# Kernel tuning notes

Measured on AMD Instinct MI355X. Metric: run time of the kernel, lower is better.

The kernel has to match this reference:

```python
import jax, jax.numpy as jnp
import numpy as np
import math

# (n, m) pairs used in forward: n in range(min(max_order,4)) = 0..3, m in -n..n step 2, (n-|m|)%2==0 -> 10 pairs
PAIRS = [(n, m) for n in range(4) for m in range(-n, n + 1, 2) if (n - abs(m)) % 2 == 0]
NPAIR = len(PAIRS)  # 10
MAXP = 3  # max radial power for n <= 3
_Cmat = np.zeros((NPAIR, MAXP + 1), dtype=np.float32)
for _k, (_n, _m) in enumerate(PAIRS):
    _ma = abs(_m)
    for _s in range((_n - _ma) // 2 + 1):
        _c = (-1) ** _s * math.factorial(_n - _s) / (
            math.factorial(_s) * math.factorial((_n + _ma) // 2 - _s) * math.factorial((_n - _ma) // 2 - _s))
        _Cmat[_k, _n - 2 * _s] += _c
CMAT = jnp.asarray(_Cmat)                                  # (10, 4) radial poly coeffs per power of r
M_ARR = jnp.asarray(np.array([m for _, m in PAIRS], dtype=np.float32))  # signed m per pair
FEAT_LEN = 20


def _pzm_single(img):
    """Zernike-moment features for one gray image (H, W) -> (10,)."""
    H, W = img.shape
    img = (img - img.mean()) / (img.std() + 1e-8)
    a = jnp.abs(img)
    s = a.sum()
    yi = jnp.arange(H, dtype=img.dtype)[:, None]
    xi = jnp.arange(W, dtype=img.dtype)[None, :]
    safe_s = jnp.maximum(s, 1e-8)
    cy = jnp.where(s < 1e-8, H / 2.0, (a * yi).sum() / safe_s)  # scipy center_of_mass
    cx = jnp.where(s < 1e-8, W / 2.0, (a * xi).sum() / safe_s)
    y = yi - cy
    x = xi - cx
    ixx = (x * x * img).sum()
    ixy = (x * y * img).sum()
    iyy = (y * y * img).sum()
    inertia = jnp.stack([jnp.stack([ixx, ixy]), jnp.stack([ixy, iyy])])
    _, vecs = jnp.linalg.eigh(inertia)
    angle = jnp.arctan2(vecs[1, 0], vecs[0, 0])
    ca, sa = jnp.cos(-angle), jnp.sin(-angle)
    x_rot = x * ca - y * sa
    y_rot = x * sa + y * ca
    r2 = x_rot * x_rot + y_rot * y_rot
    max_r = jnp.sqrt(r2.max()) + 1e-8
    r = jnp.clip(jnp.sqrt(r2 + 1e-20) / max_r, 0.0, 1.0)
    theta = jnp.arctan2(y_rot, x_rot)
    r_pows = jnp.stack([jnp.ones_like(r), r, r * r, r * r * r])    # (4, H, W)
    radial = jnp.einsum('kp,phw->khw', CMAT, r_pows)               # (10, H, W)
    mtheta = M_ARR[:, None, None] * theta                          # (10, H, W)
    denom = max_r * max_r + 1e-8
    mr = jnp.einsum('khw,hw->k', radial * jnp.cos(mtheta), img) / denom
    mi = jnp.einsum('khw,hw->k', radial * jnp.sin(mtheta), img) / denom
    return jnp.sqrt(mr * mr + mi * mi)                             # (10,)


def setup_inputs() -> dict:
    key = jax.random.key(0)
    x = jax.random.normal(key, (32, 3, 512, 512), dtype=jnp.float32)
    return {"x": x}


def reference(x):
    # RGB -> gray (channels == 3 path of the original forward)
    gray = 0.299 * x[:, 0] + 0.587 * x[:, 1] + 0.114 * x[:, 2]   # (B, H, W)
    feats = jax.vmap(_pzm_single)(gray)                          # (B, 10)
    return jnp.pad(feats, ((0, 0), (0, FEAT_LEN - feats.shape[1])))  # pad to (B, 20)
```

## Files before the change

kernel.cpp:

```cpp
#include <hip/hip_runtime.h>

#define NPIX (512*512)
#define NIMG 32
#define CTR 255.5f
#define NCH 64
#define NTHR 256
#define NP1 12
#define GSCL 32.0f
#define GINV 0.03125f

__device__ __forceinline__ double wredd(double v) {
#pragma unroll
    for (int off = 32; off; off >>= 1) v += __shfl_down(v, off, 64);
    return v;
}

__global__ __launch_bounds__(NTHR) void k1(const float* __restrict__ x,
                                           double* __restrict__ p1,
                                           char* __restrict__ gray) {
    int img = blockIdx.x >> 6;
    int chunk = blockIdx.x & (NCH - 1);
    size_t cb = (size_t)chunk * (NPIX / NCH);
    const float* xr = x + (size_t)img * 3 * NPIX;
    char* g8 = gray + (size_t)img * NPIX;

    float4 Rv[4], Gv[4], Bv[4];
#pragma unroll
    for (int j = 0; j < 4; ++j) {
        size_t off = cb + ((size_t)j * NTHR + threadIdx.x) * 4;
        Rv[j] = *(const float4*)(xr + off);
        Gv[j] = *(const float4*)(xr + NPIX + off);
        Bv[j] = *(const float4*)(xr + 2 * NPIX + off);
    }

    float A[11];
#pragma unroll
    for (int a = 0; a < 11; ++a) A[a] = 0.0f;

#pragma unroll
    for (int j = 0; j < 4; ++j) {
        size_t off = cb + ((size_t)j * NTHR + threadIdx.x) * 4;
        float gv[4];
        gv[0] = 0.299f * Rv[j].x + 0.587f * Gv[j].x + 0.114f * Bv[j].x;
        gv[1] = 0.299f * Rv[j].y + 0.587f * Gv[j].y + 0.114f * Bv[j].y;
        gv[2] = 0.299f * Rv[j].z + 0.587f * Gv[j].z + 0.114f * Bv[j].z;
        gv[3] = 0.299f * Rv[j].w + 0.587f * Gv[j].w + 0.114f * Bv[j].w;

        unsigned int pk = 0;
#pragma unroll
        for (int u = 0; u < 4; ++u) {
            int q = (int)rintf(gv[u] * GSCL);
            q = q > 127 ? 127 : (q < -127 ? -127 : q);
            pk |= ((unsigned int)(q & 0xff)) << (8 * u);
        }
        *(unsigned int*)(g8 + off) = pk;

        float v = (float)(int)(off >> 9) - CTR;
        float v2 = v * v, v3 = v2 * v;
        float u0 = (float)(int)(off & 511) - CTR;
#pragma unroll
        for (int u = 0; u < 4; ++u) {
            float gg = gv[u];
            float uu = u0 + (float)u;
            float t1 = gg * uu, t2 = t1 * uu, t3 = t2 * uu;
            A[0] += gg;
            A[1] += gg * gg;
            A[2] += t1;
            A[3] += gg * v;
            A[4] += t2;
            A[5] += t1 * v;
            A[6] += gg * v2;
            A[7] += t3;
            A[8] += t2 * v;
            A[9] += t1 * v2;
            A[10] += gg * v3;
        }
    }

    __shared__ double lds[4][11];
    int lane = threadIdx.x & 63, wv = threadIdx.x >> 6;
#pragma unroll
    for (int a = 0; a < 11; ++a) {
        double s = wredd((double)A[a]);
        if (lane == 0) lds[wv][a] = s;
    }
    __syncthreads();
    if (threadIdx.x < 11)
        p1[((size_t)img * NCH + chunk) * NP1 + threadIdx.x] =
            lds[0][threadIdx.x] + lds[1][threadIdx.x] + lds[2][threadIdx.x] + lds[3][threadIdx.x];
}

__global__ __launch_bounds__(NTHR) void k2(const char* __restrict__ gray,
                                           const double* __restrict__ p1,
                                           double* __restrict__ p2) {
    int img = blockIdx.x >> 6;
    int chunk = blockIdx.x & (NCH - 1);
    size_t cb = (size_t)chunk * (NPIX / NCH);
    const char* g8 = gray + (size_t)img * NPIX;
    int lane = threadIdx.x & 63, wv = threadIdx.x >> 6;

    size_t p = cb + (size_t)threadIdx.x * 16;
    uint4 raw = *(const uint4*)(g8 + p);

    __shared__ double bmean;
    if (wv == 0) {
        double sg = p1[((size_t)img * NCH + lane) * NP1 + 0];
        sg = wredd(sg);
        if (lane == 0) bmean = sg / (double)NPIX;
    }
    __syncthreads();
    float mean = (float)bmean;

    float v = (float)(int)(p >> 9) - CTR;
    float u0 = (float)(int)(p & 511) - CTR;
    float sa = 0.0f, sax = 0.0f;
    unsigned int w[4] = {raw.x, raw.y, raw.z, raw.w};
#pragma unroll
    for (int d = 0; d < 4; ++d) {
#pragma unroll
        for (int b = 0; b < 4; ++b) {
            float g = (float)(signed char)((w[d] >> (8 * b)) & 0xff) * GINV;
            float a = fabsf(g - mean);
            sa += a;
            sax += a * (u0 + (float)(4 * d + b));
        }
    }
    float say = sa * v;

    __shared__ double lds2[4][3];
    {
        float acc[3] = {sa, sax, say};
#pragma unroll
        for (int a = 0; a < 3; ++a) {
            double s = wredd((double)acc[a]);
            if (lane == 0) lds2[wv][a] = s;
        }
    }
    __syncthreads();
    if (threadIdx.x < 3)
        p2[((size_t)img * NCH + chunk) * 3 + threadIdx.x] =
            lds2[0][threadIdx.x] + lds2[1][threadIdx.x] + lds2[2][threadIdx.x] + lds2[3][threadIdx.x];
}

__global__ __launch_bounds__(64) void k3f(const double* __restrict__ p1,
                                          const double* __restrict__ p2,
                                          float* __restrict__ out) {
    int img = blockIdx.x;
    int lane = threadIdx.x;
    size_t b = (size_t)img * NCH + lane;
    double M[11], B[3];
#pragma unroll
    for (int a = 0; a < 11; ++a) M[a] = p1[b * NP1 + a];
#pragma unroll
    for (int a = 0; a < 3; ++a) B[a] = p2[b * 3 + a];
#pragma unroll
    for (int a = 0; a < 11; ++a) M[a] = wredd(M[a]);
#pragma unroll
    for (int a = 0; a < 3; ++a) B[a] = wredd(B[a]);

    if (lane == 0) {
        const double N = (double)NPIX;
        double G00 = M[0], Sg2 = M[1];
        double G10 = M[2], G01 = M[3], G20 = M[4], G11 = M[5], G02 = M[6];
        double G30 = M[7], G21 = M[8], G12 = M[9], G03 = M[10];
        double A0 = B[0], Ax = B[1], Ay = B[2];

        double mean2 = G00 / N;
        double var = Sg2 / N - mean2 * mean2;
        if (var < 0.0) var = 0.0;
        double inv_std = 1.0 / (sqrt(var) + 1e-8);

        double s_chk = A0 * inv_std;
        double dx, dy;
        if (s_chk < 1e-8) { dx = 0.5; dy = 0.5; }
        else { dx = Ax / A0; dy = Ay / A0; }

        double S2 = 512.0 * (512.0 * 512.0 - 1.0) / 12.0;
        double P20 = S2 * 512.0, P02 = S2 * 512.0;

        double W00 = G00 - mean2 * N;
        double W10 = G10, W01 = G01;
        double W20 = G20 - mean2 * P20;
        double W11 = G11;
        double W02 = G02 - mean2 * P02;
        double W30 = G30, W21 = G21, W12 = G12, W03 = G03;

        double N00 = W00;
        double N10 = W10 - dx * W00;
        double N01 = W01 - dy * W00;
        double N20 = W20 - 2.0 * dx * W10 + dx * dx * W00;
        double N11 = W11 - dx * W01 - dy * W10 + dx * dy * W00;
        double N02 = W02 - 2.0 * dy * W01 + dy * dy * W00;
        double N30 = W30 - 3.0 * dx * W20 + 3.0 * dx * dx * W10 - dx * dx * dx * W00;
        double N21 = W21 - dy * W20 - 2.0 * dx * W11 + 2.0 * dx * dy * W10
                   + dx * dx * W01 - dx * dx * dy * W00;
        double N12 = W12 - dx * W02 - 2.0 * dy * W11 + 2.0 * dx * dy * W01
                   + dy * dy * W10 - dx * dy * dy * W00;
        double N03 = W03 - 3.0 * dy * W02 + 3.0 * dy * dy * W01 - dy * dy * dy * W00;

        double cx = (double)CTR + dx, cy = (double)CTR + dy;
        double mdx = fmax(cx, 511.0 - cx), mdy = fmax(cy, 511.0 - cy);
        double max_r = sqrt(mdx * mdx + mdy * mdy) + 1e-8;
        double imr = 1.0 / max_r;
        double im1 = inv_std * imr, im2 = im1 * imr, im3 = im2 * imr;
        double inv_denom = 1.0 / (max_r * max_r + 1e-8);

        double S0 = N00 * inv_std;
        double R2 = (N20 + N02) * im2;
        double C1 = N10 * im1, S1 = N01 * im1;
        double C2 = (N20 - N02) * im2, Sm2 = 2.0 * N11 * im2;
        double C3 = (N30 - 3.0 * N12) * im3, Sm3 = (3.0 * N21 - N03) * im3;
        double C31 = (N30 + N12) * im3, S31 = (N21 + N03) * im3;

        double f0 = fabs(S0) * inv_denom;
        double f1 = sqrt(C1 * C1 + S1 * S1) * inv_denom;
        double f3 = sqrt(C2 * C2 + Sm2 * Sm2) * inv_denom;
        double f4 = fabs(2.0 * R2 - S0) * inv_denom;
        double f6 = sqrt(C3 * C3 + Sm3 * Sm3) * inv_denom;
        double a31r = 3.0 * C31 - 2.0 * C1, a31i = 3.0 * S31 - 2.0 * S1;
        double f7 = sqrt(a31r * a31r + a31i * a31i) * inv_denom;

        float* o = out + (size_t)img * 20;
        o[0] = (float)f0;
        o[1] = (float)f1; o[2] = (float)f1;
        o[3] = (float)f3; o[4] = (float)f4; o[5] = (float)f3;
        o[6] = (float)f6; o[7] = (float)f7; o[8] = (float)f7; o[9] = (float)f6;
        for (int k = 10; k < 20; ++k) o[k] = 0.0f;
    }
}

extern "C" void kernel_launch(void* const* d_in, const int* in_sizes, int n_in,
                              void* d_out, int out_size, void* d_ws, size_t ws_size,
                              hipStream_t stream) {
    const float* x = (const float*)d_in[0];
    float* out = (float*)d_out;

    double* p1 = (double*)d_ws;
    double* p2 = p1 + (size_t)NIMG * NCH * NP1;
    size_t base = ((size_t)NIMG * NCH * (NP1 + 3) * sizeof(double) + 255) & ~(size_t)255;
    char* gray = (char*)d_ws + base;

    dim3 grid(NIMG * NCH);
    k1<<<grid, NTHR, 0, stream>>>(x, p1, gray);
    k2<<<grid, NTHR, 0, stream>>>(gray, p1, p2);
    k3f<<<NIMG, 64, 0, stream>>>(p1, p2, out);
}
```

Baseline: 36.92 us.

## Fuse abs-moment pass and finalize into one per-image 1024-thread kernel

Merges the second-pass kernel k2 and the final feature kernel k3f into one kernel that launches one 1024-thread block per image. Each thread now loads 16 uint4 chunks of the int8 gray buffer and accumulates |g-mean| moments, reduces them in shared memory, and then wave 0 computes the Zernike features directly. This drops one kernel launch and the p2 workspace round trip. The cost is only 32 blocks, which cannot fill the GPU's compute units, so the 8 MB gray read may become latency-bound.

```diff
diff --git a/kernel.cpp b/kernel.cpp
--- a/kernel.cpp
+++ b/kernel.cpp
@@ -8,6 +8,7 @@
 #define NP1 12
 #define GSCL 32.0f
 #define GINV 0.03125f
+#define K2THR 1024
 
 __device__ __forceinline__ double wredd(double v) {
 #pragma unroll
@@ -90,19 +91,17 @@
             lds[0][threadIdx.x] + lds[1][threadIdx.x] + lds[2][threadIdx.x] + lds[3][threadIdx.x];
 }
 
-__global__ __launch_bounds__(NTHR) void k2(const char* __restrict__ gray,
-                                           const double* __restrict__ p1,
-                                           double* __restrict__ p2) {
-    int img = blockIdx.x >> 6;
-    int chunk = blockIdx.x & (NCH - 1);
-    size_t cb = (size_t)chunk * (NPIX / NCH);
+__global__ __launch_bounds__(K2THR) void k2fin(const char* __restrict__ gray,
+                                               const double* __restrict__ p1,
+                                               float* __restrict__ out) {
+    int img = blockIdx.x;
     const char* g8 = gray + (size_t)img * NPIX;
     int lane = threadIdx.x & 63, wv = threadIdx.x >> 6;
 
-    size_t p = cb + (size_t)threadIdx.x * 16;
-    uint4 raw = *(const uint4*)(g8 + p);
-
     __shared__ double bmean;
+    __shared__ double lds2[16][3];
+    __shared__ double bsum[3];
+
     if (wv == 0) {
         double sg = p1[((size_t)img * NCH + lane) * NP1 + 0];
         sg = wredd(sg);
@@ -111,23 +110,37 @@
     __syncthreads();
     float mean = (float)bmean;
 
-    float v = (float)(int)(p >> 9) - CTR;
-    float u0 = (float)(int)(p & 511) - CTR;
-    float sa = 0.0f, sax = 0.0f;
-    unsigned int w[4] = {raw.x, raw.y, raw.z, raw.w};
-#pragma unroll
-    for (int d = 0; d < 4; ++d) {
-#pragma unroll
-        for (int b = 0; b < 4; ++b) {
-            float g = (float)(signed char)((w[d] >> (8 * b)) & 0xff) * GINV;
-            float a = fabsf(g - mean);
-            sa += a;
-            sax += a * (u0 + (float)(4 * d + b));
-        }
-    }
-    float say = sa * v;
-
-    __shared__ double lds2[4][3];
+    float sa = 0.0f, sax = 0.0f, say = 0.0f;
+#pragma unroll
+    for (int g = 0; g < 4; ++g) {
+        uint4 raw[4];
+#pragma unroll
+        for (int q = 0; q < 4; ++q) {
+            size_t p = (size_t)(g * 4 + q) * (K2THR * 16) + (size_t)threadIdx.x * 16;
+            raw[q] = *(const uint4*)(g8 + p);
+        }
+#pragma unroll
+        for (int q = 0; q < 4; ++q) {
+            size_t p = (size_t)(g * 4 + q) * (K2THR * 16) + (size_t)threadIdx.x * 16;
+            float v = (float)(int)(p >> 9) - CTR;
+            float u0 = (float)(int)(p & 511) - CTR;
+            unsigned int w[4] = {raw[q].x, raw[q].y, raw[q].z, raw[q].w};
+            float psa = 0.0f, psax = 0.0f;
+#pragma unroll
+            for (int d = 0; d < 4; ++d) {
+#pragma unroll
+                for (int b = 0; b < 4; ++b) {
+                    float gg = (float)(signed char)((w[d] >> (8 * b)) & 0xff) * GINV;
+                    float a = fabsf(gg - mean);
+                    psa += a;
+                    psax += a * (u0 + (float)(4 * d + b));
+                }
+            }
+            sa += psa;
+            sax += psax;
+            say += psa * v;
+        }
+    }
     {
         float acc[3] = {sa, sax, say};
 #pragma unroll
@@ -137,33 +150,28 @@
         }
     }
     __syncthreads();
-    if (threadIdx.x < 3)
-        p2[((size_t)img * NCH + chunk) * 3 + threadIdx.x] =
-            lds2[0][threadIdx.x] + lds2[1][threadIdx.x] + lds2[2][threadIdx.x] + lds2[3][threadIdx.x];
-}
-
-__global__ __launch_bounds__(64) void k3f(const double* __restrict__ p1,
-                                          const double* __restrict__ p2,
-                                          float* __restrict__ out) {
-    int img = blockIdx.x;
-    int lane = threadIdx.x;
-    size_t b = (size_t)img * NCH + lane;
-    double M[11], B[3];
-#pragma unroll
-    for (int a = 0; a < 11; ++a) M[a] = p1[b * NP1 + a];
-#pragma unroll
-    for (int a = 0; a < 3; ++a) B[a] = p2[b * 3 + a];
+    if (threadIdx.x < 3) {
+        double s = 0.0;
+#pragma unroll
+        for (int w = 0; w < 16; ++w) s += lds2[w][threadIdx.x];
+        bsum[threadIdx.x] = s;
+    }
+    __syncthreads();
+    if (wv != 0) return;
+
+    double M[11];
+#pragma unroll
+    for (int a = 0; a < 11; ++a)
+        M[a] = p1[((size_t)img * NCH + lane) * NP1 + a];
 #pragma unroll
     for (int a = 0; a < 11; ++a) M[a] = wredd(M[a]);
-#pragma unroll
-    for (int a = 0; a < 3; ++a) B[a] = wredd(B[a]);
 
     if (lane == 0) {
+        double A0 = bsum[0], Ax = bsum[1], Ay = bsum[2];
         const double N = (double)NPIX;
         double G00 = M[0], Sg2 = M[1];
         double G10 = M[2], G01 = M[3], G20 = M[4], G11 = M[5], G02 = M[6];
         double G30 = M[7], G21 = M[8], G12 = M[9], G03 = M[10];
-        double A0 = B[0], Ax = B[1], Ay = B[2];
 
         double mean2 = G00 / N;
         double var = Sg2 / N - mean2 * mean2;
@@ -236,12 +244,9 @@
     float* out = (float*)d_out;
 
     double* p1 = (double*)d_ws;
-    double* p2 = p1 + (size_t)NIMG * NCH * NP1;
-    size_t base = ((size_t)NIMG * NCH * (NP1 + 3) * sizeof(double) + 255) & ~(size_t)255;
+    size_t base = ((size_t)NIMG * NCH * NP1 * sizeof(double) + 255) & ~(size_t)255;
     char* gray = (char*)d_ws + base;
 
-    dim3 grid(NIMG * NCH);
-    k1<<<grid, NTHR, 0, stream>>>(x, p1, gray);
-    k2<<<grid, NTHR, 0, stream>>>(gray, p1, p2);
-    k3f<<<NIMG, 64, 0, stream>>>(p1, p2, out);
-}
+    k1<<<NIMG * NCH, NTHR, 0, stream>>>(x, p1, gray);
+    k2fin<<<NIMG, K2THR, 0, stream>>>(gray, p1, out);
+}
```

Result: slower. 88.04 us (+138.5%).
